# Kernel optimization log

Measured on AMD Instinct MI355X. Metric: run time of the kernel, lower is better.

Reference implementation:

```python
import jax, jax.numpy as jnp
import numpy as np
from jax import lax

TAU = 10.0
THR = 1.0
ALPHA = float(np.exp(-1.0 / TAU))  # leak factor exp(-dt/tau), dt=1


def conv2d(x, w, pad):
    # x: [N,C,H,W], w: [O,I,kh,kw]
    return lax.conv_general_dilated(
        x, w, window_strides=(1, 1), padding=[(pad, pad), (pad, pad)],
        dimension_numbers=('NCHW', 'OIHW', 'NCHW'))


def avgpool(x, k):
    n, c, h, w = x.shape
    return x.reshape(n, c, h // k, k, w // k, k).mean(axis=(3, 5))


def exp_leak(x):
    # x: [T, ...]; v[t] = alpha*v[t-1] + x[t]; outputs membrane each step
    def step(v, xt):
        v = ALPHA * v + xt
        return v, v
    _, y = lax.scan(step, jnp.zeros_like(x[0]), x)
    return y


def lif(x):
    # LIF with SingleSpike + MembraneSubtract reset (norm_input=False)
    def step(v, xt):
        v = ALPHA * v + xt
        s = (v >= THR).astype(v.dtype)
        return v - s * THR, s
    _, s = lax.scan(step, jnp.zeros_like(x[0]), x)
    return s


def forward(x, conv1_w, conv2_w, lin_w):
    B, T = x.shape[:2]
    h = avgpool(conv2d(x.reshape(B * T, 2, 32, 32), conv1_w, 2), 4)  # [BT,4,8,8]
    h = h.reshape(B, T, 4, 8, 8).swapaxes(0, 1)                       # [T,B,4,8,8]
    h = lif(exp_leak(h)).swapaxes(0, 1).reshape(B * T, 4, 8, 8)
    h = avgpool(conv2d(h, conv2_w, 1), 2)                             # [BT,8,4,4]
    h = h.reshape(B, T, 8, 4, 4).swapaxes(0, 1)                       # [T,B,8,4,4]
    h = lif(exp_leak(h)).swapaxes(0, 1).reshape(B, T, 8 * 4 * 4)      # [B,T,128]
    return jnp.einsum('btf,of->bto', h, lin_w)                        # [B,T,2]


def setup_inputs() -> dict:
    key = jax.random.key(0)
    k1, k2, k3, k4 = jax.random.split(key, 4)
    B, T = 128, 100
    x = jax.random.uniform(k1, (B, T, 2, 32, 32), dtype=jnp.float32)
    conv1_w = jax.random.normal(k2, (4, 2, 5, 5), dtype=jnp.float32) / np.sqrt(2 * 5 * 5)
    conv2_w = jax.random.normal(k3, (8, 4, 3, 3), dtype=jnp.float32) / np.sqrt(4 * 3 * 3)
    lin_w = jax.random.normal(k4, (2, 128), dtype=jnp.float32) / np.sqrt(128)
    return {'x': x, 'conv1_w': conv1_w, 'conv2_w': conv2_w, 'lin_w': lin_w}


def reference(x, conv1_w, conv2_w, lin_w):
    return forward(x, conv1_w, conv2_w, lin_w)
```

## Files before the change

### kernel.cpp

```cpp
#include <hip/hip_runtime.h>

#define ALPHA 0.90483741803595957f

__global__ void prep_weights(const float* __restrict__ w1, const float* __restrict__ w2,
                             float* __restrict__ w1e, float* __restrict__ w2e) {
    int idx = blockIdx.x * 256 + threadIdx.x;
    if (idx < 512) {
        int v = idx & 7, u = (idx >> 3) & 7, ch = (idx >> 6) & 1, oc = idx >> 7;
        float s = 0.f;
        for (int a = 0; a < 5; ++a) {
            int i = u - a; if (i < 0 || i > 3) continue;
            for (int b = 0; b < 5; ++b) {
                int j = v - b; if (j < 0 || j > 3) continue;
                s += w1[((oc * 2 + ch) * 5 + a) * 5 + b];
            }
        }
        w1e[idx] = s * (1.f / 16.f);
    } else if (idx < 1024) {
        int k = idx - 512;
        int v = k & 3, u = (k >> 2) & 3, ch = (k >> 4) & 3, oc = k >> 6;
        float s = 0.f;
        for (int a = 0; a < 3; ++a) {
            int i = u - a; if (i < 0 || i > 1) continue;
            for (int b = 0; b < 3; ++b) {
                int j = v - b; if (j < 0 || j > 1) continue;
                s += w2[((oc * 4 + ch) * 3 + a) * 3 + b];
            }
        }
        w2e[k] = s * 0.25f;
    }
}

__global__ __launch_bounds__(256) void conv1_pool(const float* __restrict__ x,
                                                  const float* __restrict__ w1e,
                                                  float* __restrict__ y1) {
    __shared__ __align__(16) float tile[4][2][36][36];
    int tid = threadIdx.x;

    float4* t4 = (float4*)&tile[0][0][0][0];
    #pragma unroll
    for (int k = 0; k < 11; ++k) {
        int i = tid + k * 256;
        if (i < 2592) t4[i] = make_float4(0.f, 0.f, 0.f, 0.f);
    }
    __syncthreads();

    int li = tid >> 6, pos = tid & 63;
    long gi = (long)blockIdx.x * 4 + li;
    const float* src = x + gi * 2048;
    #pragma unroll
    for (int k = 0; k < 8; ++k) {
        int e = k * 256 + pos * 4;
        float4 d = *(const float4*)(src + e);
        int ch = e >> 10, rem = e & 1023, r = rem >> 5, c = rem & 31;
        float* dst = &tile[li][ch][r + 2][c + 2];
        dst[0] = d.x; dst[1] = d.y; dst[2] = d.z; dst[3] = d.w;
    }
    __syncthreads();

    int p = pos >> 3, q = pos & 7;
    float acc0 = 0.f, acc1 = 0.f, acc2 = 0.f, acc3 = 0.f;
    #pragma unroll
    for (int ch = 0; ch < 2; ++ch) {
        #pragma unroll
        for (int r = 0; r < 8; ++r) {
            const float* row = &tile[li][ch][4 * p + r][4 * q];
            float4 a = *(const float4*)row;
            float4 b = *(const float4*)(row + 4);
            float in[8] = {a.x, a.y, a.z, a.w, b.x, b.y, b.z, b.w};
            #pragma unroll
            for (int c = 0; c < 8; ++c) {
                float xi = in[c];
                acc0 += w1e[((0 * 2 + ch) * 8 + r) * 8 + c] * xi;
                acc1 += w1e[((1 * 2 + ch) * 8 + r) * 8 + c] * xi;
                acc2 += w1e[((2 * 2 + ch) * 8 + r) * 8 + c] * xi;
                acc3 += w1e[((3 * 2 + ch) * 8 + r) * 8 + c] * xi;
            }
        }
    }
    float* dst = y1 + gi * 256 + pos;
    dst[0] = acc0; dst[64] = acc1; dst[128] = acc2; dst[192] = acc3;
}

__global__ __launch_bounds__(256) void fused_rest(const float* __restrict__ y1,
                                                  const float* __restrict__ w2e,
                                                  const float* __restrict__ lw,
                                                  float* __restrict__ out) {
    __shared__ __align__(16) float spk[4][10][10];
    __shared__ __align__(16) float s2buf[2][128];
    __shared__ __align__(16) float outbuf[100][2];
    int tid = threadIdx.x;
    int b = blockIdx.x;

    for (int i = tid; i < 400; i += 256) ((float*)spk)[i] = 0.f;

    float wreg[64];
    int g = tid, oc = g >> 4, p = (g >> 2) & 3, q = g & 3;
    if (tid < 128) {
        const float4* wsrc = (const float4*)(w2e + oc * 64);
        #pragma unroll
        for (int k = 0; k < 16; ++k) {
            float4 w = wsrc[k];
            wreg[4 * k] = w.x; wreg[4 * k + 1] = w.y;
            wreg[4 * k + 2] = w.z; wreg[4 * k + 3] = w.w;
        }
    }
    int lane = tid & 63;
    float lwa = 0.f, lwb = 0.f;
    if (tid >= 128) {
        int o = (tid >> 6) - 2;
        float2 lv = *(const float2*)(lw + o * 128 + 2 * lane);
        lwa = lv.x; lwb = lv.y;
    }

    const float* yp = y1 + (long)b * 25600 + tid;
    float v1a = 0.f, v1b = 0.f, v2a = 0.f, v2b = 0.f;
    int ch = tid >> 6, r = (tid >> 3) & 7, c = tid & 7;

    float xt = yp[0];
    __syncthreads();

    for (int t = 0; t < 100; ++t) {
        float xn = (t < 99) ? yp[(t + 1) * 256] : 0.f;
        v1a = ALPHA * v1a + xt;
        v1b = ALPHA * v1b + v1a;
        float s = (v1b >= 1.f) ? 1.f : 0.f;
        v1b -= s;
        spk[ch][r + 1][c + 1] = s;
        xt = xn;
        __syncthreads();
        if (tid < 128) {
            float acc = 0.f;
            #pragma unroll
            for (int cc = 0; cc < 4; ++cc) {
                #pragma unroll
                for (int rr = 0; rr < 4; ++rr) {
                    const float* rowp = &spk[cc][2 * p + rr][2 * q];
                    float2 a = *(const float2*)rowp;
                    float2 bb = *(const float2*)(rowp + 2);
                    int wb = cc * 16 + rr * 4;
                    acc += wreg[wb] * a.x + wreg[wb + 1] * a.y
                         + wreg[wb + 2] * bb.x + wreg[wb + 3] * bb.y;
                }
            }
            v2a = ALPHA * v2a + acc;
            v2b = ALPHA * v2b + v2a;
            float s2 = (v2b >= 1.f) ? 1.f : 0.f;
            v2b -= s2;
            s2buf[t & 1][g] = s2;
        } else if (t > 0) {
            float2 sv = *(const float2*)&s2buf[(t - 1) & 1][2 * lane];
            float pa = sv.x * lwa + sv.y * lwb;
            #pragma unroll
            for (int off = 32; off; off >>= 1) pa += __shfl_down(pa, off);
            if (lane == 0) outbuf[t - 1][(tid >> 6) - 2] = pa;
        }
        __syncthreads();
    }
    if (tid >= 128) {
        float2 sv = *(const float2*)&s2buf[1][2 * lane];
        float pa = sv.x * lwa + sv.y * lwb;
        #pragma unroll
        for (int off = 32; off; off >>= 1) pa += __shfl_down(pa, off);
        if (lane == 0) outbuf[99][(tid >> 6) - 2] = pa;
    }
    __syncthreads();
    float* op = out + (long)b * 200;
    if (tid < 200) op[tid] = ((float*)outbuf)[tid];
}

extern "C" void kernel_launch(void* const* d_in, const int* in_sizes, int n_in,
                              void* d_out, int out_size, void* d_ws, size_t ws_size,
                              hipStream_t stream) {
    const float* x  = (const float*)d_in[0];
    const float* w1 = (const float*)d_in[1];
    const float* w2 = (const float*)d_in[2];
    const float* lw = (const float*)d_in[3];
    float* out = (float*)d_out;

    float* ws  = (float*)d_ws;
    float* w1e = ws;
    float* w2e = ws + 512;
    float* y1  = ws + 1024;

    prep_weights<<<4, 256, 0, stream>>>(w1, w2, w1e, w2e);
    conv1_pool<<<3200, 256, 0, stream>>>(x, w1e, y1);
    fused_rest<<<128, 256, 0, stream>>>(y1, w2e, lw, out);
}
```

Before: 231.3 us.

## Shrink recurrent kernel to one wavefront and split conv1 work across more blocks

The sequential time-loop kernel now runs as a single 64-lane wavefront per batch element. Each lane handles four layer-1 neurons and two layer-2 output channels, so barriers are cheap and fewer warps are stalled. The final linear layer is moved out of the loop: layer-2 spikes for all timesteps are stored in shared memory and reduced once at the end. Conv1 now handles two images per block, with each wave computing two output channels, which doubles the block count for better occupancy. In exchange, per-lane register pressure and serial work per step go up in the recurrent kernel.

New measurement: 243.7 us. +5.4%, slower.

```diff
diff --git a/kernel.cpp b/kernel.cpp
--- a/kernel.cpp
+++ b/kernel.cpp
@@ -34,139 +34,155 @@
 __global__ __launch_bounds__(256) void conv1_pool(const float* __restrict__ x,
                                                   const float* __restrict__ w1e,
                                                   float* __restrict__ y1) {
-    __shared__ __align__(16) float tile[4][2][36][36];
+    __shared__ __align__(16) float tile[2][2][36][36];
     int tid = threadIdx.x;
 
     float4* t4 = (float4*)&tile[0][0][0][0];
     #pragma unroll
-    for (int k = 0; k < 11; ++k) {
+    for (int k = 0; k < 6; ++k) {
         int i = tid + k * 256;
-        if (i < 2592) t4[i] = make_float4(0.f, 0.f, 0.f, 0.f);
+        if (i < 1296) t4[i] = make_float4(0.f, 0.f, 0.f, 0.f);
     }
     __syncthreads();
 
-    int li = tid >> 6, pos = tid & 63;
-    long gi = (long)blockIdx.x * 4 + li;
-    const float* src = x + gi * 2048;
-    #pragma unroll
-    for (int k = 0; k < 8; ++k) {
-        int e = k * 256 + pos * 4;
+    long gi0 = (long)blockIdx.x * 2;
+    int simg = tid >> 7, soff = tid & 127;
+    const float* src = x + (gi0 + simg) * 2048;
+    #pragma unroll
+    for (int k = 0; k < 4; ++k) {
+        int e = k * 512 + soff * 4;
         float4 d = *(const float4*)(src + e);
         int ch = e >> 10, rem = e & 1023, r = rem >> 5, c = rem & 31;
-        float* dst = &tile[li][ch][r + 2][c + 2];
-        dst[0] = d.x; dst[1] = d.y; dst[2] = d.z; dst[3] = d.w;
+        float* dst = &tile[simg][ch][r + 2][c + 2];
+        *(float2*)dst = make_float2(d.x, d.y);
+        *(float2*)(dst + 2) = make_float2(d.z, d.w);
     }
     __syncthreads();
 
-    int p = pos >> 3, q = pos & 7;
-    float acc0 = 0.f, acc1 = 0.f, acc2 = 0.f, acc3 = 0.f;
+    int w = tid >> 6, im = w >> 1, ocp = w & 1;
+    int pos = tid & 63, p = pos >> 3, q = pos & 7;
+    float acc0 = 0.f, acc1 = 0.f;
+    const float* wb = w1e + ocp * 256;
     #pragma unroll
     for (int ch = 0; ch < 2; ++ch) {
         #pragma unroll
         for (int r = 0; r < 8; ++r) {
-            const float* row = &tile[li][ch][4 * p + r][4 * q];
+            const float* row = &tile[im][ch][4 * p + r][4 * q];
             float4 a = *(const float4*)row;
             float4 b = *(const float4*)(row + 4);
-            float in[8] = {a.x, a.y, a.z, a.w, b.x, b.y, b.z, b.w};
+            const float* w0 = wb + ch * 64 + r * 8;
+            const float* w1 = w0 + 128;
+            acc0 += w0[0] * a.x + w0[1] * a.y + w0[2] * a.z + w0[3] * a.w
+                  + w0[4] * b.x + w0[5] * b.y + w0[6] * b.z + w0[7] * b.w;
+            acc1 += w1[0] * a.x + w1[1] * a.y + w1[2] * a.z + w1[3] * a.w
+                  + w1[4] * b.x + w1[5] * b.y + w1[6] * b.z + w1[7] * b.w;
+        }
+    }
+    float* dst = y1 + (gi0 + im) * 256 + ocp * 128 + pos;
+    dst[0] = acc0; dst[64] = acc1;
+}
+
+__global__ __launch_bounds__(64) void fused_rest(const float* __restrict__ y1,
+                                                 const float* __restrict__ w2e,
+                                                 const float* __restrict__ lw,
+                                                 float* __restrict__ out) {
+    __shared__ __align__(16) float spk[4][10][12];
+    __shared__ __align__(16) float s2all[100][132];
+    __shared__ __align__(16) float lwl[256];
+    int lane = threadIdx.x;
+    int b = blockIdx.x;
+
+    for (int i = lane; i < 480; i += 64) ((float*)spk)[i] = 0.f;
+    ((float4*)lwl)[lane] = ((const float4*)lw)[lane];
+
+    float wr0[64], wr1[64];
+    {
+        const float4* ws0 = (const float4*)(w2e + (lane >> 4) * 64);
+        const float4* ws1 = (const float4*)(w2e + ((lane >> 4) + 4) * 64);
+        #pragma unroll
+        for (int k = 0; k < 16; ++k) {
+            float4 a = ws0[k];
+            wr0[4 * k] = a.x; wr0[4 * k + 1] = a.y; wr0[4 * k + 2] = a.z; wr0[4 * k + 3] = a.w;
+            float4 c = ws1[k];
+            wr1[4 * k] = c.x; wr1[4 * k + 1] = c.y; wr1[4 * k + 2] = c.z; wr1[4 * k + 3] = c.w;
+        }
+    }
+
+    int r1 = (lane >> 3) & 7, c1 = lane & 7;
+    int p = (lane >> 2) & 3, q = lane & 3;
+    const float* yp = y1 + (long)b * 25600 + lane;
+
+    float v1a[4] = {0.f, 0.f, 0.f, 0.f}, v1b[4] = {0.f, 0.f, 0.f, 0.f};
+    float v2a0 = 0.f, v2b0 = 0.f, v2a1 = 0.f, v2b1 = 0.f;
+    float xt[4];
+    #pragma unroll
+    for (int k = 0; k < 4; ++k) xt[k] = yp[k * 64];
+    __syncthreads();
+
+    for (int t = 0; t < 100; ++t) {
+        float xn[4];
+        if (t < 99) {
+            const float* ypn = yp + (t + 1) * 256;
             #pragma unroll
-            for (int c = 0; c < 8; ++c) {
-                float xi = in[c];
-                acc0 += w1e[((0 * 2 + ch) * 8 + r) * 8 + c] * xi;
-                acc1 += w1e[((1 * 2 + ch) * 8 + r) * 8 + c] * xi;
-                acc2 += w1e[((2 * 2 + ch) * 8 + r) * 8 + c] * xi;
-                acc3 += w1e[((3 * 2 + ch) * 8 + r) * 8 + c] * xi;
+            for (int k = 0; k < 4; ++k) xn[k] = ypn[k * 64];
+        } else {
+            #pragma unroll
+            for (int k = 0; k < 4; ++k) xn[k] = 0.f;
+        }
+        #pragma unroll
+        for (int k = 0; k < 4; ++k) {
+            v1a[k] = ALPHA * v1a[k] + xt[k];
+            v1b[k] = ALPHA * v1b[k] + v1a[k];
+            float s = (v1b[k] >= 1.f) ? 1.f : 0.f;
+            v1b[k] -= s;
+            spk[k][r1 + 1][c1 + 1] = s;
+            xt[k] = xn[k];
+        }
+        __syncthreads();
+
+        float acc0 = 0.f, acc1 = 0.f;
+        #pragma unroll
+        for (int cc = 0; cc < 4; ++cc) {
+            #pragma unroll
+            for (int rr = 0; rr < 4; ++rr) {
+                const float* rowp = &spk[cc][2 * p + rr][2 * q];
+                float2 a = *(const float2*)rowp;
+                float2 bb = *(const float2*)(rowp + 2);
+                int wx = cc * 16 + rr * 4;
+                acc0 += wr0[wx] * a.x + wr0[wx + 1] * a.y + wr0[wx + 2] * bb.x + wr0[wx + 3] * bb.y;
+                acc1 += wr1[wx] * a.x + wr1[wx + 1] * a.y + wr1[wx + 2] * bb.x + wr1[wx + 3] * bb.y;
             }
         }
-    }
-    float* dst = y1 + gi * 256 + pos;
-    dst[0] = acc0; dst[64] = acc1; dst[128] = acc2; dst[192] = acc3;
-}
-
-__global__ __launch_bounds__(256) void fused_rest(const float* __restrict__ y1,
-                                                  const float* __restrict__ w2e,
-                                                  const float* __restrict__ lw,
-                                                  float* __restrict__ out) {
-    __shared__ __align__(16) float spk[4][10][10];
-    __shared__ __align__(16) float s2buf[2][128];
-    __shared__ __align__(16) float outbuf[100][2];
-    int tid = threadIdx.x;
-    int b = blockIdx.x;
-
-    for (int i = tid; i < 400; i += 256) ((float*)spk)[i] = 0.f;
-
-    float wreg[64];
-    int g = tid, oc = g >> 4, p = (g >> 2) & 3, q = g & 3;
-    if (tid < 128) {
-        const float4* wsrc = (const float4*)(w2e + oc * 64);
-        #pragma unroll
-        for (int k = 0; k < 16; ++k) {
-            float4 w = wsrc[k];
-            wreg[4 * k] = w.x; wreg[4 * k + 1] = w.y;
-            wreg[4 * k + 2] = w.z; wreg[4 * k + 3] = w.w;
-        }
-    }
-    int lane = tid & 63;
-    float lwa = 0.f, lwb = 0.f;
-    if (tid >= 128) {
-        int o = (tid >> 6) - 2;
-        float2 lv = *(const float2*)(lw + o * 128 + 2 * lane);
-        lwa = lv.x; lwb = lv.y;
-    }
-
-    const float* yp = y1 + (long)b * 25600 + tid;
-    float v1a = 0.f, v1b = 0.f, v2a = 0.f, v2b = 0.f;
-    int ch = tid >> 6, r = (tid >> 3) & 7, c = tid & 7;
-
-    float xt = yp[0];
-    __syncthreads();
-
-    for (int t = 0; t < 100; ++t) {
-        float xn = (t < 99) ? yp[(t + 1) * 256] : 0.f;
-        v1a = ALPHA * v1a + xt;
-        v1b = ALPHA * v1b + v1a;
-        float s = (v1b >= 1.f) ? 1.f : 0.f;
-        v1b -= s;
-        spk[ch][r + 1][c + 1] = s;
-        xt = xn;
+        v2a0 = ALPHA * v2a0 + acc0; v2b0 = ALPHA * v2b0 + v2a0;
+        float s0 = (v2b0 >= 1.f) ? 1.f : 0.f; v2b0 -= s0;
+        v2a1 = ALPHA * v2a1 + acc1; v2b1 = ALPHA * v2b1 + v2a1;
+        float s1 = (v2b1 >= 1.f) ? 1.f : 0.f; v2b1 -= s1;
+        s2all[t][lane] = s0;
+        s2all[t][lane + 64] = s1;
         __syncthreads();
-        if (tid < 128) {
-            float acc = 0.f;
-            #pragma unroll
-            for (int cc = 0; cc < 4; ++cc) {
-                #pragma unroll
-                for (int rr = 0; rr < 4; ++rr) {
-                    const float* rowp = &spk[cc][2 * p + rr][2 * q];
-                    float2 a = *(const float2*)rowp;
-                    float2 bb = *(const float2*)(rowp + 2);
-                    int wb = cc * 16 + rr * 4;
-                    acc += wreg[wb] * a.x + wreg[wb + 1] * a.y
-                         + wreg[wb + 2] * bb.x + wreg[wb + 3] * bb.y;
-                }
-            }
-            v2a = ALPHA * v2a + acc;
-            v2b = ALPHA * v2b + v2a;
-            float s2 = (v2b >= 1.f) ? 1.f : 0.f;
-            v2b -= s2;
-            s2buf[t & 1][g] = s2;
-        } else if (t > 0) {
-            float2 sv = *(const float2*)&s2buf[(t - 1) & 1][2 * lane];
-            float pa = sv.x * lwa + sv.y * lwb;
-            #pragma unroll
-            for (int off = 32; off; off >>= 1) pa += __shfl_down(pa, off);
-            if (lane == 0) outbuf[t - 1][(tid >> 6) - 2] = pa;
-        }
-        __syncthreads();
-    }
-    if (tid >= 128) {
-        float2 sv = *(const float2*)&s2buf[1][2 * lane];
-        float pa = sv.x * lwa + sv.y * lwb;
-        #pragma unroll
-        for (int off = 32; off; off >>= 1) pa += __shfl_down(pa, off);
-        if (lane == 0) outbuf[99][(tid >> 6) - 2] = pa;
-    }
-    __syncthreads();
+    }
+
+    int tb = lane + 64;
+    const float4* sa = (const float4*)&s2all[lane][0];
+    const float4* sb = (const float4*)&s2all[(tb < 100) ? tb : 0][0];
+    const float4* lw4 = (const float4*)lwl;
+    float o00 = 0.f, o01 = 0.f, o10 = 0.f, o11 = 0.f;
+    #pragma unroll
+    for (int k = 0; k < 32; ++k) {
+        float4 w0 = lw4[k], w1 = lw4[32 + k];
+        float4 A = sa[k], B = sb[k];
+        o00 += A.x * w0.x + A.y * w0.y + A.z * w0.z + A.w * w0.w;
+        o01 += A.x * w1.x + A.y * w1.y + A.z * w1.z + A.w * w1.w;
+        o10 += B.x * w0.x + B.y * w0.y + B.z * w0.z + B.w * w0.w;
+        o11 += B.x * w1.x + B.y * w1.y + B.z * w1.z + B.w * w1.w;
+    }
     float* op = out + (long)b * 200;
-    if (tid < 200) op[tid] = ((float*)outbuf)[tid];
+    op[lane * 2] = o00;
+    op[lane * 2 + 1] = o01;
+    if (tb < 100) {
+        op[tb * 2] = o10;
+        op[tb * 2 + 1] = o11;
+    }
 }
 
 extern "C" void kernel_launch(void* const* d_in, const int* in_sizes, int n_in,
@@ -184,6 +200,6 @@
     float* y1  = ws + 1024;
 
     prep_weights<<<4, 256, 0, stream>>>(w1, w2, w1e, w2e);
-    conv1_pool<<<3200, 256, 0, stream>>>(x, w1e, y1);
-    fused_rest<<<128, 256, 0, stream>>>(y1, w2e, lw, out);
-}
+    conv1_pool<<<6400, 256, 0, stream>>>(x, w1e, y1);
+    fused_rest<<<128, 64, 0, stream>>>(y1, w2e, lw, out);
+}
```

## Stage conv1 weights in LDS and restructure recurrent kernel with deferred linear readout

Applied to the files above, without the earlier changes.

conv1_pool now copies the folded conv1 weights into shared memory, laid out so each row of weights loads as float4 vectors. It also pads the input tile and drops the second barrier, relying on each wavefront reading only the tile it wrote. fused_rest shrinks to 128 threads, each running two layer-1 LIF neurons and one layer-2 neuron. It stores every layer-2 spike in shared memory and does the linear readout once after the time loop, instead of using dedicated warps and shuffle reductions every step. This takes work off the serial per-timestep path and removes idle threads, at the cost of more shared memory and an intra-wave LDS ordering assumption.

Result: faster. 218.1 us (-5.7%).

```diff
diff --git a/kernel.cpp b/kernel.cpp
--- a/kernel.cpp
+++ b/kernel.cpp
@@ -34,139 +34,141 @@
 __global__ __launch_bounds__(256) void conv1_pool(const float* __restrict__ x,
                                                   const float* __restrict__ w1e,
                                                   float* __restrict__ y1) {
-    __shared__ __align__(16) float tile[4][2][36][36];
+    __shared__ __align__(16) float tile[4][2][36][40];
+    __shared__ __align__(16) float wlds[512];
     int tid = threadIdx.x;
 
     float4* t4 = (float4*)&tile[0][0][0][0];
     #pragma unroll
-    for (int k = 0; k < 11; ++k) {
+    for (int k = 0; k < 12; ++k) {
         int i = tid + k * 256;
-        if (i < 2592) t4[i] = make_float4(0.f, 0.f, 0.f, 0.f);
+        if (i < 2880) t4[i] = make_float4(0.f, 0.f, 0.f, 0.f);
+    }
+    for (int j = tid; j < 512; j += 256) {
+        int oc = j >> 7, ch = (j >> 6) & 1, r = (j >> 3) & 7, c = j & 7;
+        wlds[((ch * 8 + r) * 4 + oc) * 8 + c] = w1e[j];
     }
     __syncthreads();
 
-    int li = tid >> 6, pos = tid & 63;
-    long gi = (long)blockIdx.x * 4 + li;
+    int w = tid >> 6, lane = tid & 63;
+    long gi = (long)blockIdx.x * 4 + w;
     const float* src = x + gi * 2048;
     #pragma unroll
     for (int k = 0; k < 8; ++k) {
-        int e = k * 256 + pos * 4;
+        int e = k * 256 + lane * 4;
         float4 d = *(const float4*)(src + e);
         int ch = e >> 10, rem = e & 1023, r = rem >> 5, c = rem & 31;
-        float* dst = &tile[li][ch][r + 2][c + 2];
-        dst[0] = d.x; dst[1] = d.y; dst[2] = d.z; dst[3] = d.w;
+        float* dst = &tile[w][ch][r + 2][c + 2];
+        *(float2*)dst = make_float2(d.x, d.y);
+        *(float2*)(dst + 2) = make_float2(d.z, d.w);
     }
-    __syncthreads();
 
-    int p = pos >> 3, q = pos & 7;
+    int p = lane >> 3, q = lane & 7;
     float acc0 = 0.f, acc1 = 0.f, acc2 = 0.f, acc3 = 0.f;
     #pragma unroll
     for (int ch = 0; ch < 2; ++ch) {
         #pragma unroll
         for (int r = 0; r < 8; ++r) {
-            const float* row = &tile[li][ch][4 * p + r][4 * q];
+            const float* row = &tile[w][ch][4 * p + r][4 * q];
             float4 a = *(const float4*)row;
             float4 b = *(const float4*)(row + 4);
-            float in[8] = {a.x, a.y, a.z, a.w, b.x, b.y, b.z, b.w};
-            #pragma unroll
-            for (int c = 0; c < 8; ++c) {
-                float xi = in[c];
-                acc0 += w1e[((0 * 2 + ch) * 8 + r) * 8 + c] * xi;
-                acc1 += w1e[((1 * 2 + ch) * 8 + r) * 8 + c] * xi;
-                acc2 += w1e[((2 * 2 + ch) * 8 + r) * 8 + c] * xi;
-                acc3 += w1e[((3 * 2 + ch) * 8 + r) * 8 + c] * xi;
-            }
+            const float* wr = &wlds[(ch * 8 + r) * 32];
+            float4 wa, wb;
+            wa = *(const float4*)(wr + 0);  wb = *(const float4*)(wr + 4);
+            acc0 += wa.x * a.x + wa.y * a.y + wa.z * a.z + wa.w * a.w
+                  + wb.x * b.x + wb.y * b.y + wb.z * b.z + wb.w * b.w;
+            wa = *(const float4*)(wr + 8);  wb = *(const float4*)(wr + 12);
+            acc1 += wa.x * a.x + wa.y * a.y + wa.z * a.z + wa.w * a.w
+                  + wb.x * b.x + wb.y * b.y + wb.z * b.z + wb.w * b.w;
+            wa = *(const float4*)(wr + 16); wb = *(const float4*)(wr + 20);
+            acc2 += wa.x * a.x + wa.y * a.y + wa.z * a.z + wa.w * a.w
+                  + wb.x * b.x + wb.y * b.y + wb.z * b.z + wb.w * b.w;
+            wa = *(const float4*)(wr + 24); wb = *(const float4*)(wr + 28);
+            acc3 += wa.x * a.x + wa.y * a.y + wa.z * a.z + wa.w * a.w
+                  + wb.x * b.x + wb.y * b.y + wb.z * b.z + wb.w * b.w;
         }
     }
-    float* dst = y1 + gi * 256 + pos;
+    float* dst = y1 + gi * 256 + lane;
     dst[0] = acc0; dst[64] = acc1; dst[128] = acc2; dst[192] = acc3;
 }
 
-__global__ __launch_bounds__(256) void fused_rest(const float* __restrict__ y1,
-                                                  const float* __restrict__ w2e,
-                                                  const float* __restrict__ lw,
-                                                  float* __restrict__ out) {
-    __shared__ __align__(16) float spk[4][10][10];
-    __shared__ __align__(16) float s2buf[2][128];
-    __shared__ __align__(16) float outbuf[100][2];
+__global__ __launch_bounds__(128, 1) void fused_rest(const float* __restrict__ y1,
+                                                     const float* __restrict__ w2e,
+                                                     const float* __restrict__ lw,
+                                                     float* __restrict__ out) {
+    __shared__ __align__(16) float spk[4][10][12];
+    __shared__ __align__(16) float s2all[100][132];
+    __shared__ __align__(16) float lwl[256];
     int tid = threadIdx.x;
     int b = blockIdx.x;
 
-    for (int i = tid; i < 400; i += 256) ((float*)spk)[i] = 0.f;
+    for (int i = tid; i < 480; i += 128) ((float*)spk)[i] = 0.f;
+    ((float2*)lwl)[tid] = ((const float2*)lw)[tid];
 
-    float wreg[64];
-    int g = tid, oc = g >> 4, p = (g >> 2) & 3, q = g & 3;
-    if (tid < 128) {
-        const float4* wsrc = (const float4*)(w2e + oc * 64);
-        #pragma unroll
-        for (int k = 0; k < 16; ++k) {
-            float4 w = wsrc[k];
-            wreg[4 * k] = w.x; wreg[4 * k + 1] = w.y;
-            wreg[4 * k + 2] = w.z; wreg[4 * k + 3] = w.w;
-        }
-    }
-    int lane = tid & 63;
-    float lwa = 0.f, lwb = 0.f;
-    if (tid >= 128) {
-        int o = (tid >> 6) - 2;
-        float2 lv = *(const float2*)(lw + o * 128 + 2 * lane);
-        lwa = lv.x; lwb = lv.y;
-    }
+    int oc = tid >> 4, p = (tid >> 2) & 3, q = tid & 3;
+    const float4* wp = (const float4*)(w2e + oc * 64);
+    float4 w00 = wp[0],  w01 = wp[1],  w02 = wp[2],  w03 = wp[3];
+    float4 w04 = wp[4],  w05 = wp[5],  w06 = wp[6],  w07 = wp[7];
+    float4 w08 = wp[8],  w09 = wp[9],  w10 = wp[10], w11 = wp[11];
+    float4 w12 = wp[12], w13 = wp[13], w14 = wp[14], w15 = wp[15];
 
+    int ch1 = tid >> 6, r1 = (tid >> 3) & 7, c1 = tid & 7;
     const float* yp = y1 + (long)b * 25600 + tid;
-    float v1a = 0.f, v1b = 0.f, v2a = 0.f, v2b = 0.f;
-    int ch = tid >> 6, r = (tid >> 3) & 7, c = tid & 7;
-
-    float xt = yp[0];
+    float v1a0 = 0.f, v1b0 = 0.f, v1a1 = 0.f, v1b1 = 0.f;
+    float v2a = 0.f, v2b = 0.f;
+    float xt0 = yp[0], xt1 = yp[128];
     __syncthreads();
 
+#define C2(cc, rr, W, P) { const float* rowp = &spk[cc][2 * p + (rr)][2 * q];      \
+        float2 a_ = *(const float2*)rowp; float2 b_ = *(const float2*)(rowp + 2);  \
+        P += W.x * a_.x + W.y * a_.y + W.z * b_.x + W.w * b_.y; }
+
     for (int t = 0; t < 100; ++t) {
-        float xn = (t < 99) ? yp[(t + 1) * 256] : 0.f;
-        v1a = ALPHA * v1a + xt;
-        v1b = ALPHA * v1b + v1a;
-        float s = (v1b >= 1.f) ? 1.f : 0.f;
-        v1b -= s;
-        spk[ch][r + 1][c + 1] = s;
-        xt = xn;
+        float xn0 = 0.f, xn1 = 0.f;
+        if (t < 99) {
+            const float* ypn = yp + (t + 1) * 256;
+            xn0 = ypn[0]; xn1 = ypn[128];
+        }
+        v1a0 = ALPHA * v1a0 + xt0; v1b0 = ALPHA * v1b0 + v1a0;
+        float s0 = (v1b0 >= 1.f) ? 1.f : 0.f; v1b0 -= s0;
+        spk[ch1][r1 + 1][c1 + 1] = s0;
+        v1a1 = ALPHA * v1a1 + xt1; v1b1 = ALPHA * v1b1 + v1a1;
+        float s1 = (v1b1 >= 1.f) ? 1.f : 0.f; v1b1 -= s1;
+        spk[ch1 + 2][r1 + 1][c1 + 1] = s1;
+        xt0 = xn0; xt1 = xn1;
         __syncthreads();
-        if (tid < 128) {
-            float acc = 0.f;
-            #pragma unroll
-            for (int cc = 0; cc < 4; ++cc) {
-                #pragma unroll
-                for (int rr = 0; rr < 4; ++rr) {
-                    const float* rowp = &spk[cc][2 * p + rr][2 * q];
-                    float2 a = *(const float2*)rowp;
-                    float2 bb = *(const float2*)(rowp + 2);
-                    int wb = cc * 16 + rr * 4;
-                    acc += wreg[wb] * a.x + wreg[wb + 1] * a.y
-                         + wreg[wb + 2] * bb.x + wreg[wb + 3] * bb.y;
-                }
-            }
-            v2a = ALPHA * v2a + acc;
-            v2b = ALPHA * v2b + v2a;
-            float s2 = (v2b >= 1.f) ? 1.f : 0.f;
-            v2b -= s2;
-            s2buf[t & 1][g] = s2;
-        } else if (t > 0) {
-            float2 sv = *(const float2*)&s2buf[(t - 1) & 1][2 * lane];
-            float pa = sv.x * lwa + sv.y * lwb;
-            #pragma unroll
-            for (int off = 32; off; off >>= 1) pa += __shfl_down(pa, off);
-            if (lane == 0) outbuf[t - 1][(tid >> 6) - 2] = pa;
-        }
+
+        float p0 = 0.f, p1 = 0.f, p2 = 0.f, p3 = 0.f;
+        C2(0, 0, w00, p0) C2(0, 1, w01, p0) C2(0, 2, w02, p0) C2(0, 3, w03, p0)
+        C2(1, 0, w04, p1) C2(1, 1, w05, p1) C2(1, 2, w06, p1) C2(1, 3, w07, p1)
+        C2(2, 0, w08, p2) C2(2, 1, w09, p2) C2(2, 2, w10, p2) C2(2, 3, w11, p2)
+        C2(3, 0, w12, p3) C2(3, 1, w13, p3) C2(3, 2, w14, p3) C2(3, 3, w15, p3)
+        float acc = (p0 + p1) + (p2 + p3);
+
+        v2a = ALPHA * v2a + acc; v2b = ALPHA * v2b + v2a;
+        float ss = (v2b >= 1.f) ? 1.f : 0.f; v2b -= ss;
+        s2all[t][tid] = ss;
         __syncthreads();
     }
-    if (tid >= 128) {
-        float2 sv = *(const float2*)&s2buf[1][2 * lane];
-        float pa = sv.x * lwa + sv.y * lwb;
+#undef C2
+
+    if (tid < 100) {
+        const float4* sa  = (const float4*)&s2all[tid][0];
+        const float4* lw4 = (const float4*)lwl;
+        float e0a = 0.f, e0b = 0.f, e1a = 0.f, e1b = 0.f;
         #pragma unroll
-        for (int off = 32; off; off >>= 1) pa += __shfl_down(pa, off);
-        if (lane == 0) outbuf[99][(tid >> 6) - 2] = pa;
+        for (int k = 0; k < 32; k += 2) {
+            float4 A = sa[k], B = sa[k + 1];
+            float4 u0 = lw4[k], u1 = lw4[k + 1];
+            float4 v0 = lw4[32 + k], v1 = lw4[33 + k];
+            e0a += A.x * u0.x + A.y * u0.y + A.z * u0.z + A.w * u0.w;
+            e0b += B.x * u1.x + B.y * u1.y + B.z * u1.z + B.w * u1.w;
+            e1a += A.x * v0.x + A.y * v0.y + A.z * v0.z + A.w * v0.w;
+            e1b += B.x * v1.x + B.y * v1.y + B.z * v1.z + B.w * v1.w;
+        }
+        float2 res = make_float2(e0a + e0b, e1a + e1b);
+        *(float2*)(out + (long)b * 200 + tid * 2) = res;
     }
-    __syncthreads();
-    float* op = out + (long)b * 200;
-    if (tid < 200) op[tid] = ((float*)outbuf)[tid];
 }
 
 extern "C" void kernel_launch(void* const* d_in, const int* in_sizes, int n_in,
@@ -185,5 +187,5 @@
 
     prep_weights<<<4, 256, 0, stream>>>(w1, w2, w1e, w2e);
     conv1_pool<<<3200, 256, 0, stream>>>(x, w1e, y1);
-    fused_rest<<<128, 256, 0, stream>>>(y1, w2e, lw, out);
+    fused_rest<<<128, 128, 0, stream>>>(y1, w2e, lw, out);
 }
```
